# Optimization experiments

Measured on AMD Instinct MI355X. Metric: run time of the kernel, lower is better.

The kernel has to match this reference:

```python
import jax, jax.numpy as jnp
import numpy as np

TAU = 1.1      # LIF membrane time constant
ALPHA = 4.0    # sigmoid surrogate sharpness (spikingjelly default)
EPS = 1e-5     # BatchNorm eps
SCALE = 0.125  # attention scale


def lif(x, v_th):
    # Single-step LIF, v init 0, decay_input=True: v = x / tau; spike = H(v - v_th)
    # Straight-through: forward heaviside, backward sigmoid surrogate derivative.
    u = x / TAU - v_th
    sg = jax.nn.sigmoid(ALPHA * u)
    return sg + jax.lax.stop_gradient((u >= 0.0).astype(x.dtype) - sg)


def bn(x, gamma, beta):
    # BatchNorm1d in training mode on [B, C, N]: stats over (B, N) per channel
    mean = jnp.mean(x, axis=(0, 2), keepdims=True)
    var = jnp.var(x, axis=(0, 2), keepdims=True)
    return gamma[None, :, None] * (x - mean) * jax.lax.rsqrt(var + EPS) + beta[None, :, None]


def conv1x1(w, x):
    # Conv1d kernel_size=1: pointwise channel mix, x: [B,C,N], w: [O,C]
    return jnp.einsum('oc,bcn->bon', w, x)


def setup_inputs() -> dict:
    key = jax.random.key(0)
    B, C, N = 32, 512, 1024
    ks = jax.random.split(key, 6)
    s = 1.0 / np.sqrt(C)
    inp = {"x": jax.random.normal(ks[0], (B, C, N), jnp.float32)}
    for name, k in zip(["q", "k", "v", "proj"], ks[1:5]):
        inp[name + "_w"] = jax.random.uniform(k, (C, C), jnp.float32, -s, s)
        inp[name + "_gamma"] = jnp.ones((C,), jnp.float32)
        inp[name + "_beta"] = jnp.zeros((C,), jnp.float32)
    inp["proj_b"] = jax.random.uniform(ks[5], (C,), jnp.float32, -s, s)
    return inp


def reference(x, q_w, q_gamma, q_beta, k_w, k_gamma, k_beta, v_w, v_gamma, v_beta,
              proj_w, proj_b, proj_gamma, proj_beta):
    # x: [B, C, N]
    q = lif(bn(conv1x1(q_w, x), q_gamma, q_beta), 1.0)  # [B,C,N] spikes
    k = lif(bn(conv1x1(k_w, x), k_gamma, k_beta), 1.0)
    v = lif(bn(conv1x1(v_w, x), v_gamma, v_beta), 1.0)
    # linear (softmax-free) attention: kv[c,d] = sum_n k[n,c] v[n,d]
    kv = jnp.einsum('bcn,bdn->bcd', k, v)               # [B,C,C]
    attn = jnp.einsum('bcn,bcd->bdn', q, kv) * SCALE    # [B,C,N] (already transposed back)
    attn = lif(attn, 0.5)
    out = conv1x1(proj_w, attn) + proj_b[None, :, None]
    return lif(bn(out, proj_gamma, proj_beta), 1.0)
```

## Files before the change

### kernel.cpp

```cpp
#include <hip/hip_runtime.h>
#include <cstddef>


#define CC 512
#define BB 32
#define NN 1024

typedef __attribute__((ext_vector_type(4))) float v4f;
typedef __attribute__((ext_vector_type(2))) float v2f;
typedef __attribute__((ext_vector_type(4))) int v4i;
typedef __attribute__((ext_vector_type(8))) int v8i;
typedef unsigned char uchar;
typedef unsigned long long ull;

__device__ __forceinline__ uchar f2e4s(float v) {
  const uchar s = (v < 0.f) ? 0x80 : 0x00;
  float a = fabsf(v);
  if (a >= 464.f) return s | 0x7E;
  if (a < 0.015625f) {
    int q = (int)rintf(a * 512.f);
    return s | (uchar)q;
  }
  const int e = (int)((__float_as_uint(a) >> 23) & 0xFF) - 126;
  const float scale = __uint_as_float((unsigned)(4 - e + 127) << 23);
  const int q = (int)rintf(a * scale);
  int code = ((e - 1 + 7) << 3) + (q - 8);
  if (code > 0x7E) code = 0x7E;
  return s | (uchar)code;
}
__device__ __forceinline__ float e42f(uchar b) {
  const int e = (b >> 3) & 15, m = b & 7;
  const float mag = e ? __uint_as_float((unsigned)((e + 120) << 23) | ((unsigned)m << 20))
                      : (float)m * 0.001953125f;
  return (b & 0x80) ? -mag : mag;
}

__device__ __forceinline__ unsigned pk4_fp8(float a0, float a1, float a2, float a3) {
#if __has_builtin(__builtin_amdgcn_cvt_pk_fp8_f32)
  int r = __builtin_amdgcn_cvt_pk_fp8_f32(a0, a1, 0, false);
  r = __builtin_amdgcn_cvt_pk_fp8_f32(a2, a3, r, true);
  return (unsigned)r;
#else
  return (unsigned)f2e4s(a0) | ((unsigned)f2e4s(a1) << 8) |
         ((unsigned)f2e4s(a2) << 16) | ((unsigned)f2e4s(a3) << 24);
#endif
}
__device__ __forceinline__ uchar enc1(float v) {
#if __has_builtin(__builtin_amdgcn_cvt_pk_fp8_f32)
  return (uchar)(__builtin_amdgcn_cvt_pk_fp8_f32(v, v, 0, false) & 0xFF);
#else
  return f2e4s(v);
#endif
}
template <bool HI>
__device__ __forceinline__ v2f dec2(int src) {
#if __has_builtin(__builtin_amdgcn_cvt_pk_f32_fp8)
  return __builtin_amdgcn_cvt_pk_f32_fp8(src, HI);
#else
  v2f r;
  const int s = HI ? (src >> 16) : src;
  r[0] = e42f((uchar)s);
  r[1] = e42f((uchar)(s >> 8));
  return r;
#endif
}

__device__ __forceinline__ void gload16(const void* g, void* l) {
  __builtin_amdgcn_global_load_lds(
      (const __attribute__((address_space(1))) unsigned int*)g,
      (__attribute__((address_space(3))) unsigned int*)l, 16, 0, 0);
}

__device__ __forceinline__ float2 chan_affine(const float* __restrict__ P, int c,
                                              float g, float bt) {
  const float* pc = P + (size_t)c * 16;
  float S = 0.f, Q = 0.f;
#pragma unroll
  for (int t = 0; t < 8; t++) { S += pc[2 * t]; Q += pc[2 * t + 1]; }
  const float mean = S * (1.f / 32768.f);
  const float var = fmaxf(Q * (1.f / 32768.f) - mean * mean, 0.f);
  const float rinv = 1.f / sqrtf(var + 1e-5f);
  const float a = g * rinv;
  return make_float2(a, bt - mean * a);
}

template <int EPI>
__global__ __launch_bounds__(256) void gemm8(const uchar* __restrict__ A,
                                             const uchar* __restrict__ B,
                                             uchar* __restrict__ Cout,
                                             const float* __restrict__ bias,
                                             int M, int N, int K,
                                             long sA, long sB, long sC) {
  __shared__ __align__(16) uchar lds[32768];
  const int b = blockIdx.z;
  const uchar* Ab = A + (size_t)b * sA;
  const uchar* Bb = B + (size_t)b * sB;
  const int m0 = blockIdx.y * 128, n0 = blockIdx.x * 128;
  const int tid = threadIdx.x;
  const int wave = tid >> 6, lane = tid & 63;
  const int lrow = lane & 15, lquad = lane >> 4;
  const int wr = wave >> 1, wc = wave & 1;

  v4f acc[4][4];
#pragma unroll
  for (int i = 0; i < 4; i++)
#pragma unroll
    for (int j = 0; j < 4; j++) acc[i][j] = (v4f)0.f;

  const uchar* gA0 = Ab + (size_t)(m0 + 32 * wave + lrow) * K + lquad * 32;
  const uchar* gA1 = gA0 + (size_t)16 * K;
  const uchar* gB0 = Bb + (size_t)(n0 + 32 * wave + lrow) * K + lquad * 32;
  const uchar* gB1 = gB0 + (size_t)16 * K;
  uchar* lA0 = lds + (2 * wave) * 2048;
  uchar* lA1 = lA0 + 2048;
  uchar* lB0 = lds + 16384 + (2 * wave) * 2048;
  uchar* lB1 = lB0 + 2048;

  for (int k0 = 0; k0 < K; k0 += 128) {
    gload16(gA0, lA0);
    gload16(gA0 + 16, lA0 + 1024);
    gload16(gA1, lA1);
    gload16(gA1 + 16, lA1 + 1024);
    gload16(gB0, lB0);
    gload16(gB0 + 16, lB0 + 1024);
    gload16(gB1, lB1);
    gload16(gB1 + 16, lB1 + 1024);
    gA0 += 128; gA1 += 128; gB0 += 128; gB1 += 128;
    __syncthreads();
    const uchar* ra = lds + (size_t)(4 * wr) * 2048 + 16 * lane;
    const uchar* rb = lds + 16384 + (size_t)(4 * wc) * 2048 + 16 * lane;
    v8i af[4], bf[4];
#pragma unroll
    for (int i = 0; i < 4; i++) {
      const v4i lo = *(const v4i*)(ra + i * 2048);
      const v4i hi = *(const v4i*)(ra + i * 2048 + 1024);
      af[i][0] = lo[0]; af[i][1] = lo[1]; af[i][2] = lo[2]; af[i][3] = lo[3];
      af[i][4] = hi[0]; af[i][5] = hi[1]; af[i][6] = hi[2]; af[i][7] = hi[3];
    }
#pragma unroll
    for (int j = 0; j < 4; j++) {
      const v4i lo = *(const v4i*)(rb + j * 2048);
      const v4i hi = *(const v4i*)(rb + j * 2048 + 1024);
      bf[j][0] = lo[0]; bf[j][1] = lo[1]; bf[j][2] = lo[2]; bf[j][3] = lo[3];
      bf[j][4] = hi[0]; bf[j][5] = hi[1]; bf[j][6] = hi[2]; bf[j][7] = hi[3];
    }
#pragma unroll
    for (int i = 0; i < 4; i++)
#pragma unroll
      for (int j = 0; j < 4; j++)
        acc[i][j] = __builtin_amdgcn_mfma_scale_f32_16x16x128_f8f6f4(
            af[i], bf[j], acc[i][j], 0, 0, 0, 127, 0, 127);
    __syncthreads();
  }

  if (EPI == 3) {
#pragma unroll
    for (int mi = 0; mi < 4; mi++)
#pragma unroll
      for (int r = 0; r < 4; r++) {
        const float bi = bias[m0 + 64 * wr + 16 * mi + lquad * 4 + r];
#pragma unroll
        for (int ni = 0; ni < 4; ni++) acc[mi][ni][r] += bi;
      }
  }

#pragma unroll
  for (int mi = 0; mi < 4; mi++) {
    const int row0 = m0 + 64 * wr + 16 * mi + lquad * 4;
#pragma unroll
    for (int ni = 0; ni < 4; ni++) {
      const int col = n0 + 64 * wc + 16 * ni + lrow;
      uchar* cp = Cout + (size_t)b * sC + (size_t)row0 * N + col;
      if (EPI == 1) {
#pragma unroll
        for (int r = 0; r < 4; r++) {
          const float u = (acc[mi][ni][r] * 0.125f) / 1.1f - 0.5f;
          cp[(size_t)r * N] = (u >= 0.f) ? (uchar)0x38 : (uchar)0;
        }
      } else {
        const unsigned pk = pk4_fp8(acc[mi][ni][0], acc[mi][ni][1],
                                    acc[mi][ni][2], acc[mi][ni][3]);
#pragma unroll
        for (int r = 0; r < 4; r++) cp[(size_t)r * N] = (uchar)(pk >> (8 * r));
      }
    }
  }
}

__global__ __launch_bounds__(256) void stats_part8_k(const uchar* __restrict__ in,
                                                     float* __restrict__ P,
                                                     long bstride) {
  const int part = blockIdx.x, c = blockIdx.y;
  const int tid = threadIdx.x;
  const int bi = part * 4 + (tid >> 6);
  const int lane = tid & 63;
  const uchar* p = in + (size_t)bi * bstride + (size_t)c * 1024 + lane * 16;
  const uint4 u = *(const uint4*)p;
  const int w4[4] = {(int)u.x, (int)u.y, (int)u.z, (int)u.w};
  float s = 0.f, s2 = 0.f;
#pragma unroll
  for (int t = 0; t < 4; t++) {
    const v2f a = dec2<false>(w4[t]);
    const v2f bb = dec2<true>(w4[t]);
    s += (a[0] + a[1]) + (bb[0] + bb[1]);
    s2 += a[0] * a[0] + a[1] * a[1] + bb[0] * bb[0] + bb[1] * bb[1];
  }
#pragma unroll
  for (int off = 32; off > 0; off >>= 1) {
    s += __shfl_down(s, off, 64);
    s2 += __shfl_down(s2, off, 64);
  }
  __shared__ float rs[4], rq[4];
  const int w = tid >> 6;
  if (lane == 0) { rs[w] = s; rq[w] = s2; }
  __syncthreads();
  if (tid == 0) {
    float2 o = make_float2(rs[0] + rs[1] + rs[2] + rs[3],
                           rq[0] + rq[1] + rq[2] + rq[3]);
    *(float2*)(P + (size_t)(c * 8 + part) * 2) = o;
  }
}

__global__ __launch_bounds__(256) void apply_all_k(const uchar* __restrict__ qkv8,
                                                   uchar* __restrict__ q8,
                                                   uchar* __restrict__ k8,
                                                   uchar* __restrict__ v8,
                                                   const float* __restrict__ P,
                                                   const float* __restrict__ qg, const float* __restrict__ qb,
                                                   const float* __restrict__ kg, const float* __restrict__ kb,
                                                   const float* __restrict__ vg, const float* __restrict__ vb) {
  const int bid = blockIdx.x;
  const int tid = threadIdx.x;
  if (bid < 16384) {
    __shared__ uchar tile[32][33];
    const int nb = bid & 31, cb = (bid >> 5) & 15, b = bid >> 9;
    const int n0 = nb * 32, c0 = cb * 32;
    const uchar* in = qkv8 + (size_t)b * (1536 * 1024);
    const int cl = tid >> 3;
    const int n4 = (tid & 7) * 4;
    const int c = c0 + cl;
    const float2 ab = chan_affine(P, c, qg[c], qb[c]);
    const unsigned w = *(const unsigned*)(in + (size_t)c * 1024 + n0 + n4);
    const v2f a = dec2<false>((int)w);
    const v2f bb = dec2<true>((int)w);
    tile[cl][n4 + 0] = (ab.x * a[0] + ab.y >= 1.1f) ? (uchar)0x38 : (uchar)0;
    tile[cl][n4 + 1] = (ab.x * a[1] + ab.y >= 1.1f) ? (uchar)0x38 : (uchar)0;
    tile[cl][n4 + 2] = (ab.x * bb[0] + ab.y >= 1.1f) ? (uchar)0x38 : (uchar)0;
    tile[cl][n4 + 3] = (ab.x * bb[1] + ab.y >= 1.1f) ? (uchar)0x38 : (uchar)0;
    __syncthreads();
    uchar* out = q8 + (size_t)b * (NN * CC);
    const int nl = tid >> 3;
    const int cq = (tid & 7) * 4;
    uchar4 v;
    v.x = tile[cq][nl]; v.y = tile[cq + 1][nl];
    v.z = tile[cq + 2][nl]; v.w = tile[cq + 3][nl];
    *(uchar4*)(out + (size_t)(n0 + nl) * CC + c0 + cq) = v;
  } else {
    const int t0 = bid - 16384;
    const int sec = t0 >> 13;
    const int blk = t0 & 8191;
    const size_t t = (size_t)blk * 256 + tid;
    const size_t i = t * 8;
    const int b = (int)(i >> 19);
    const int rem = (int)(i & 524287);
    const int c = rem >> 10, n = rem & 1023;
    const int cg = 512 + 512 * sec + c;
    const float2 ab = chan_affine(P, cg, sec ? vg[c] : kg[c], sec ? vb[c] : kb[c]);
    const uchar* src = qkv8 + (size_t)b * (1536 * 1024) + (size_t)cg * 1024 + n;
    const uint2 u = *(const uint2*)src;
    ull packed = 0;
    {
      const v2f a = dec2<false>((int)u.x);
      const v2f bb = dec2<true>((int)u.x);
      const float f[4] = {a[0], a[1], bb[0], bb[1]};
#pragma unroll
      for (int j = 0; j < 4; j++)
        packed |= ((ab.x * f[j] + ab.y >= 1.1f) ? 0x38ull : 0ull) << (8 * j);
    }
    {
      const v2f a = dec2<false>((int)u.y);
      const v2f bb = dec2<true>((int)u.y);
      const float f[4] = {a[0], a[1], bb[0], bb[1]};
#pragma unroll
      for (int j = 0; j < 4; j++)
        packed |= ((ab.x * f[j] + ab.y >= 1.1f) ? 0x38ull : 0ull) << (8 * (4 + j));
    }
    uchar* dst = (sec ? v8 : k8) + (size_t)b * (CC * NN) + (size_t)c * 1024 + n;
    *(ull*)dst = packed;
  }
}

__global__ __launch_bounds__(256) void apply_final_k(const uchar* __restrict__ in,
                                                     float* __restrict__ outp,
                                                     const float* __restrict__ Pp,
                                                     const float* __restrict__ pg,
                                                     const float* __restrict__ pb) {
  const size_t idx = ((size_t)blockIdx.x * 256 + threadIdx.x) * 8;
  const int c = (int)((idx >> 10) & (CC - 1));
  const float2 ab = chan_affine(Pp, c, pg[c], pb[c]);
  const uint2 u = *(const uint2*)(in + idx);
  float of[8];
  {
    const v2f a = dec2<false>((int)u.x);
    const v2f bb = dec2<true>((int)u.x);
    of[0] = (ab.x * a[0] + ab.y >= 1.1f) ? 1.f : 0.f;
    of[1] = (ab.x * a[1] + ab.y >= 1.1f) ? 1.f : 0.f;
    of[2] = (ab.x * bb[0] + ab.y >= 1.1f) ? 1.f : 0.f;
    of[3] = (ab.x * bb[1] + ab.y >= 1.1f) ? 1.f : 0.f;
  }
  {
    const v2f a = dec2<false>((int)u.y);
    const v2f bb = dec2<true>((int)u.y);
    of[4] = (ab.x * a[0] + ab.y >= 1.1f) ? 1.f : 0.f;
    of[5] = (ab.x * a[1] + ab.y >= 1.1f) ? 1.f : 0.f;
    of[6] = (ab.x * bb[0] + ab.y >= 1.1f) ? 1.f : 0.f;
    of[7] = (ab.x * bb[1] + ab.y >= 1.1f) ? 1.f : 0.f;
  }
  float* op = outp + idx;
  *(float4*)op = make_float4(of[0], of[1], of[2], of[3]);
  *(float4*)(op + 4) = make_float4(of[4], of[5], of[6], of[7]);
}

__global__ __launch_bounds__(256) void prep_k(const float* __restrict__ x,
                                              const float* __restrict__ w0, const float* __restrict__ w1,
                                              const float* __restrict__ w2, const float* __restrict__ w3,
                                              uchar* __restrict__ xT8,
                                              uchar* __restrict__ o0, uchar* __restrict__ o1,
                                              uchar* __restrict__ o2, uchar* __restrict__ o3) {
  const int bid = blockIdx.x;
  const int tid = threadIdx.x;
  if (bid < 16384) {
    __shared__ uchar tile[32][33];
    const int nb = bid & 31, cb = (bid >> 5) & 15, b = bid >> 9;
    const int n0 = nb * 32, c0 = cb * 32;
    const float* in = x + (size_t)b * (CC * NN);
    const int tx = tid & 31, ty = tid >> 5;
#pragma unroll
    for (int i = 0; i < 32; i += 8) {
      tile[ty + i][tx] = enc1(in[(size_t)(c0 + ty + i) * NN + n0 + tx]);
    }
    __syncthreads();
    uchar* o = xT8 + (size_t)b * (NN * CC);
    const int nl = tid >> 3;
    const int cq = (tid & 7) * 4;
    uchar4 v;
    v.x = tile[cq][nl]; v.y = tile[cq + 1][nl];
    v.z = tile[cq + 2][nl]; v.w = tile[cq + 3][nl];
    *(uchar4*)(o + (size_t)(n0 + nl) * CC + c0 + cq) = v;
  } else {
    const int t = bid - 16384;
    const int mat = t >> 8, blk = t & 255;
    const float* src = (mat == 0) ? w0 : (mat == 1) ? w1 : (mat == 2) ? w2 : w3;
    uchar* dst = (mat == 0) ? o0 : (mat == 1) ? o1 : (mat == 2) ? o2 : o3;
    const int i = (blk * 256 + tid) * 4;
    float4 v = *(const float4*)(src + i);
    *(unsigned*)(dst + i) = pk4_fp8(v.x, v.y, v.z, v.w);
  }
}

extern "C" void kernel_launch(void* const* d_in, const int* in_sizes, int n_in,
                              void* d_out, int out_size, void* d_ws, size_t ws_size,
                              hipStream_t stream) {
  const float* x          = (const float*)d_in[0];
  const float* q_w        = (const float*)d_in[1];
  const float* q_gamma    = (const float*)d_in[2];
  const float* q_beta     = (const float*)d_in[3];
  const float* k_w        = (const float*)d_in[4];
  const float* k_gamma    = (const float*)d_in[5];
  const float* k_beta     = (const float*)d_in[6];
  const float* v_w        = (const float*)d_in[7];
  const float* v_gamma    = (const float*)d_in[8];
  const float* v_beta     = (const float*)d_in[9];
  const float* proj_w     = (const float*)d_in[10];
  const float* proj_gamma = (const float*)d_in[11];
  const float* proj_beta  = (const float*)d_in[12];
  const float* proj_b     = (const float*)d_in[13];

  char* base = (char*)d_ws;
  const size_t MB = 1u << 20;
  uchar*  xT8    = (uchar*)base;
  uchar*  qkv8   = (uchar*)(base + 16 * MB);
  uchar*  q8     = (uchar*)(base + 64 * MB);
  uchar*  k8     = (uchar*)(base + 80 * MB);
  uchar*  v8     = (uchar*)(base + 96 * MB);
  uchar*  kvT8   = (uchar*)(base + 112 * MB);
  uchar*  attnT8 = (uchar*)(base + 120 * MB);
  uchar*  outpre8= (uchar*)(base + 136 * MB);
  uchar*  wqkv8  = (uchar*)(base + 152 * MB);
  uchar*  wp8    = wqkv8 + 3 * CC * CC;
  float*  P      = (float*)(base + 154 * MB);
  float*  Pp     = P + 1536 * 16;
  float* dout = (float*)d_out;

  const long QKVL = (long)3 * CC * NN;
  const long NCL  = (long)NN * CC;
  const long CNL  = (long)CC * NN;
  const long KVL  = (long)CC * CC;

  prep_k<<<17408, 256, 0, stream>>>(x, q_w, k_w, v_w, proj_w, xT8,
                                    wqkv8, wqkv8 + CC * CC, wqkv8 + 2 * CC * CC, wp8);

  gemm8<2><<<dim3(NN / 128, 1536 / 128, BB), 256, 0, stream>>>(
      wqkv8, xT8, qkv8, nullptr, 1536, NN, CC, 0, NCL, QKVL);

  stats_part8_k<<<dim3(8, 1536), 256, 0, stream>>>(qkv8, P, QKVL);

  apply_all_k<<<32768, 256, 0, stream>>>(qkv8, q8, k8, v8, P,
                                         q_gamma, q_beta, k_gamma, k_beta,
                                         v_gamma, v_beta);

  gemm8<0><<<dim3(CC / 128, CC / 128, BB), 256, 0, stream>>>(
      v8, k8, kvT8, nullptr, CC, CC, NN, CNL, CNL, KVL);
  gemm8<1><<<dim3(CC / 128, NN / 128, BB), 256, 0, stream>>>(
      q8, kvT8, attnT8, nullptr, NN, CC, CC, NCL, KVL, NCL);
  gemm8<3><<<dim3(NN / 128, CC / 128, BB), 256, 0, stream>>>(
      wp8, attnT8, outpre8, proj_b, CC, NN, CC, 0, NCL, CNL);

  stats_part8_k<<<dim3(8, CC), 256, 0, stream>>>(outpre8, Pp, CNL);
  apply_final_k<<<8192, 256, 0, stream>>>(outpre8, dout, Pp, proj_gamma, proj_beta);
}
```

Before: 322.1 us.

## Add 256x256-tile ping-pong FP8 GEMM kernel for QKV, attention and projection GEMMs

Introduces a new gemm8p kernel with 512 threads and 256x256 output tiles. It double-buffers 128-wide K slices in 128 KB of LDS and interleaves global-to-LDS loads with MFMA phases, using barriers and priority bumps. Three of the four GEMMs now use it to raise data reuse per tile and overlap memory with compute. The larger LDS footprint and tiles cut occupancy and the number of workgroups, which may hurt load balance on the smaller GEMMs.

```diff
diff --git a/kernel.cpp b/kernel.cpp
--- a/kernel.cpp
+++ b/kernel.cpp
@@ -167,6 +167,145 @@
 #pragma unroll
   for (int mi = 0; mi < 4; mi++) {
     const int row0 = m0 + 64 * wr + 16 * mi + lquad * 4;
+#pragma unroll
+    for (int ni = 0; ni < 4; ni++) {
+      const int col = n0 + 64 * wc + 16 * ni + lrow;
+      uchar* cp = Cout + (size_t)b * sC + (size_t)row0 * N + col;
+      if (EPI == 1) {
+#pragma unroll
+        for (int r = 0; r < 4; r++) {
+          const float u = (acc[mi][ni][r] * 0.125f) / 1.1f - 0.5f;
+          cp[(size_t)r * N] = (u >= 0.f) ? (uchar)0x38 : (uchar)0;
+        }
+      } else {
+        const unsigned pk = pk4_fp8(acc[mi][ni][0], acc[mi][ni][1],
+                                    acc[mi][ni][2], acc[mi][ni][3]);
+#pragma unroll
+        for (int r = 0; r < 4; r++) cp[(size_t)r * N] = (uchar)(pk >> (8 * r));
+      }
+    }
+  }
+}
+
+template <int EPI>
+__global__ __launch_bounds__(512, 2) void gemm8p(const uchar* __restrict__ A,
+                                                 const uchar* __restrict__ B,
+                                                 uchar* __restrict__ Cout,
+                                                 const float* __restrict__ bias,
+                                                 int M, int N, int K,
+                                                 long sA, long sB, long sC) {
+  __shared__ __align__(16) uchar lds[131072];
+  const int b = blockIdx.z;
+  const uchar* Ab = A + (size_t)b * sA;
+  const uchar* Bb = B + (size_t)b * sB;
+  const int m0 = blockIdx.y * 256, n0 = blockIdx.x * 256;
+  const int tid = threadIdx.x;
+  const int wave = tid >> 6, lane = tid & 63;
+  const int lrow = lane & 15, lquad = lane >> 4;
+  const int wr = wave >> 2, wc = wave & 3;
+
+  v4f acc[8][4];
+#pragma unroll
+  for (int i = 0; i < 8; i++)
+#pragma unroll
+    for (int j = 0; j < 4; j++) acc[i][j] = (v4f)0.f;
+
+  const uchar* gA0 = Ab + (size_t)(m0 + 32 * wave + lrow) * K + lquad * 32;
+  const uchar* gA1 = gA0 + (size_t)16 * K;
+  const uchar* gB0 = Bb + (size_t)(n0 + 32 * wave + lrow) * K + lquad * 32;
+  const uchar* gB1 = gB0 + (size_t)16 * K;
+
+  const int NT = K >> 7;
+
+#define SSA_STAGE_A(bufi)                                   \
+  do {                                                      \
+    uchar* la = lds + (bufi) * 65536 + (2 * wave) * 2048;   \
+    gload16(gA0, la);                                       \
+    gload16(gA0 + 16, la + 1024);                           \
+    gload16(gA1, la + 2048);                                \
+    gload16(gA1 + 16, la + 3072);                           \
+  } while (0)
+#define SSA_STAGE_B(bufi)                                   \
+  do {                                                      \
+    uchar* lb = lds + (bufi) * 65536 + 32768 + (2 * wave) * 2048; \
+    gload16(gB0, lb);                                       \
+    gload16(gB0 + 16, lb + 1024);                           \
+    gload16(gB1, lb + 2048);                                \
+    gload16(gB1 + 16, lb + 3072);                           \
+  } while (0)
+
+  SSA_STAGE_A(0);
+  SSA_STAGE_B(0);
+  gA0 += 128; gA1 += 128; gB0 += 128; gB1 += 128;
+  asm volatile("s_waitcnt vmcnt(0)" ::: "memory");
+  __builtin_amdgcn_s_barrier();
+
+  for (int kt = 0; kt < NT; ++kt) {
+    const int cur = kt & 1;
+    const int nxt = cur ^ 1;
+    const bool more = (kt + 1 < NT);
+    const uchar* raA = lds + cur * 65536 + (8 * wr) * 2048 + 16 * lane;
+    const uchar* raB = lds + cur * 65536 + 32768 + (4 * wc) * 2048 + 16 * lane;
+    v8i bf[4];
+#pragma unroll
+    for (int p = 0; p < 4; ++p) {
+      const uchar* ra = raA + (2 * p) * 2048;
+      const v4i a0lo = *(const v4i*)(ra);
+      const v4i a0hi = *(const v4i*)(ra + 1024);
+      const v4i a1lo = *(const v4i*)(ra + 2048);
+      const v4i a1hi = *(const v4i*)(ra + 3072);
+      if (p == 0) {
+#pragma unroll
+        for (int j = 0; j < 4; ++j) {
+          const v4i lo = *(const v4i*)(raB + j * 2048);
+          const v4i hi = *(const v4i*)(raB + j * 2048 + 1024);
+          bf[j][0] = lo[0]; bf[j][1] = lo[1]; bf[j][2] = lo[2]; bf[j][3] = lo[3];
+          bf[j][4] = hi[0]; bf[j][5] = hi[1]; bf[j][6] = hi[2]; bf[j][7] = hi[3];
+        }
+        if (more) SSA_STAGE_A(nxt);
+      }
+      if (p == 1 && more) {
+        SSA_STAGE_B(nxt);
+        gA0 += 128; gA1 += 128; gB0 += 128; gB1 += 128;
+      }
+      __builtin_amdgcn_s_barrier();
+      asm volatile("s_waitcnt lgkmcnt(0)" ::: "memory");
+      __builtin_amdgcn_sched_barrier(0);
+      __builtin_amdgcn_s_setprio(1);
+      v8i af0, af1;
+      af0[0] = a0lo[0]; af0[1] = a0lo[1]; af0[2] = a0lo[2]; af0[3] = a0lo[3];
+      af0[4] = a0hi[0]; af0[5] = a0hi[1]; af0[6] = a0hi[2]; af0[7] = a0hi[3];
+      af1[0] = a1lo[0]; af1[1] = a1lo[1]; af1[2] = a1lo[2]; af1[3] = a1lo[3];
+      af1[4] = a1hi[0]; af1[5] = a1hi[1]; af1[6] = a1hi[2]; af1[7] = a1hi[3];
+#pragma unroll
+      for (int j = 0; j < 4; ++j) {
+        acc[2 * p][j] = __builtin_amdgcn_mfma_scale_f32_16x16x128_f8f6f4(
+            af0, bf[j], acc[2 * p][j], 0, 0, 0, 127, 0, 127);
+        acc[2 * p + 1][j] = __builtin_amdgcn_mfma_scale_f32_16x16x128_f8f6f4(
+            af1, bf[j], acc[2 * p + 1][j], 0, 0, 0, 127, 0, 127);
+      }
+      __builtin_amdgcn_s_setprio(0);
+      if (p == 3 && more) asm volatile("s_waitcnt vmcnt(0)" ::: "memory");
+      __builtin_amdgcn_s_barrier();
+    }
+  }
+#undef SSA_STAGE_A
+#undef SSA_STAGE_B
+
+  if (EPI == 3) {
+#pragma unroll
+    for (int mi = 0; mi < 8; mi++)
+#pragma unroll
+      for (int r = 0; r < 4; r++) {
+        const float bi = bias[m0 + 128 * wr + 16 * mi + lquad * 4 + r];
+#pragma unroll
+        for (int ni = 0; ni < 4; ni++) acc[mi][ni][r] += bi;
+      }
+  }
+
+#pragma unroll
+  for (int mi = 0; mi < 8; mi++) {
+    const int row0 = m0 + 128 * wr + 16 * mi + lquad * 4;
 #pragma unroll
     for (int ni = 0; ni < 4; ni++) {
       const int col = n0 + 64 * wc + 16 * ni + lrow;
@@ -400,7 +539,7 @@
   prep_k<<<17408, 256, 0, stream>>>(x, q_w, k_w, v_w, proj_w, xT8,
                                     wqkv8, wqkv8 + CC * CC, wqkv8 + 2 * CC * CC, wp8);
 
-  gemm8<2><<<dim3(NN / 128, 1536 / 128, BB), 256, 0, stream>>>(
+  gemm8p<2><<<dim3(NN / 256, 1536 / 256, BB), 512, 0, stream>>>(
       wqkv8, xT8, qkv8, nullptr, 1536, NN, CC, 0, NCL, QKVL);
 
   stats_part8_k<<<dim3(8, 1536), 256, 0, stream>>>(qkv8, P, QKVL);
@@ -411,9 +550,9 @@
 
   gemm8<0><<<dim3(CC / 128, CC / 128, BB), 256, 0, stream>>>(
       v8, k8, kvT8, nullptr, CC, CC, NN, CNL, CNL, KVL);
-  gemm8<1><<<dim3(CC / 128, NN / 128, BB), 256, 0, stream>>>(
+  gemm8p<1><<<dim3(CC / 256, NN / 256, BB), 512, 0, stream>>>(
       q8, kvT8, attnT8, nullptr, NN, CC, CC, NCL, KVL, NCL);
-  gemm8<3><<<dim3(NN / 128, CC / 128, BB), 256, 0, stream>>>(
+  gemm8p<3><<<dim3(NN / 256, CC / 256, BB), 512, 0, stream>>>(
       wp8, attnT8, outpre8, proj_b, CC, NN, CC, 0, NCL, CNL);
 
   stats_part8_k<<<dim3(8, CC), 256, 0, stream>>>(outpre8, Pp, CNL);
```

After: 313.1 us. -2.8%, faster.

## Double-buffer LDS tiles in FP8 GEMM with vmcnt-based prefetch and MFMA priority

Applied to the files above, without the earlier changes.

Converts the FP8 MFMA GEMM from a single-buffered load-sync-compute loop to a two-stage LDS ping-pong. The next K tile is prefetched while the current one is computed, with waits done through a partial s_waitcnt vmcnt instead of full __syncthreads. It also raises wave priority around the MFMA block. LDS per block doubles to 64 KB, which may reduce occupancy, and the hand-counted vmcnt relies on the exact number of outstanding loads.

```diff
diff --git a/kernel.cpp b/kernel.cpp
--- a/kernel.cpp
+++ b/kernel.cpp
@@ -85,13 +85,13 @@
 }
 
 template <int EPI>
-__global__ __launch_bounds__(256) void gemm8(const uchar* __restrict__ A,
-                                             const uchar* __restrict__ B,
-                                             uchar* __restrict__ Cout,
-                                             const float* __restrict__ bias,
-                                             int M, int N, int K,
-                                             long sA, long sB, long sC) {
-  __shared__ __align__(16) uchar lds[32768];
+__global__ __launch_bounds__(256) void gemm8q(const uchar* __restrict__ A,
+                                              const uchar* __restrict__ B,
+                                              uchar* __restrict__ Cout,
+                                              const float* __restrict__ bias,
+                                              int M, int N, int K,
+                                              long sA, long sB, long sC) {
+  __shared__ __align__(16) uchar lds[65536];
   const int b = blockIdx.z;
   const uchar* Ab = A + (size_t)b * sA;
   const uchar* Bb = B + (size_t)b * sB;
@@ -111,24 +111,37 @@
   const uchar* gA1 = gA0 + (size_t)16 * K;
   const uchar* gB0 = Bb + (size_t)(n0 + 32 * wave + lrow) * K + lquad * 32;
   const uchar* gB1 = gB0 + (size_t)16 * K;
-  uchar* lA0 = lds + (2 * wave) * 2048;
-  uchar* lA1 = lA0 + 2048;
-  uchar* lB0 = lds + 16384 + (2 * wave) * 2048;
-  uchar* lB1 = lB0 + 2048;
-
-  for (int k0 = 0; k0 < K; k0 += 128) {
-    gload16(gA0, lA0);
-    gload16(gA0 + 16, lA0 + 1024);
-    gload16(gA1, lA1);
-    gload16(gA1 + 16, lA1 + 1024);
-    gload16(gB0, lB0);
-    gload16(gB0 + 16, lB0 + 1024);
-    gload16(gB1, lB1);
-    gload16(gB1 + 16, lB1 + 1024);
+
+  const int NT = K >> 7;
+
+  auto stage = [&](int bufi) {
+    uchar* la = lds + bufi * 32768 + (2 * wave) * 2048;
+    uchar* lb = la + 16384;
+    gload16(gA0, la);
+    gload16(gA0 + 16, la + 1024);
+    gload16(gA1, la + 2048);
+    gload16(gA1 + 16, la + 3072);
+    gload16(gB0, lb);
+    gload16(gB0 + 16, lb + 1024);
+    gload16(gB1, lb + 2048);
+    gload16(gB1 + 16, lb + 3072);
     gA0 += 128; gA1 += 128; gB0 += 128; gB1 += 128;
-    __syncthreads();
-    const uchar* ra = lds + (size_t)(4 * wr) * 2048 + 16 * lane;
-    const uchar* rb = lds + 16384 + (size_t)(4 * wc) * 2048 + 16 * lane;
+  };
+
+  stage(0);
+  if (NT > 1) stage(1);
+
+  for (int kt = 0; kt < NT; ++kt) {
+    const int cur = kt & 1;
+    if (kt + 1 < NT) {
+      asm volatile("s_waitcnt vmcnt(8)" ::: "memory");
+    } else {
+      asm volatile("s_waitcnt vmcnt(0)" ::: "memory");
+    }
+    __builtin_amdgcn_s_barrier();
+
+    const uchar* ra = lds + cur * 32768 + (size_t)(4 * wr) * 2048 + 16 * lane;
+    const uchar* rb = lds + cur * 32768 + 16384 + (size_t)(4 * wc) * 2048 + 16 * lane;
     v8i af[4], bf[4];
 #pragma unroll
     for (int i = 0; i < 4; i++) {
@@ -144,13 +157,19 @@
       bf[j][0] = lo[0]; bf[j][1] = lo[1]; bf[j][2] = lo[2]; bf[j][3] = lo[3];
       bf[j][4] = hi[0]; bf[j][5] = hi[1]; bf[j][6] = hi[2]; bf[j][7] = hi[3];
     }
+    __builtin_amdgcn_s_setprio(1);
 #pragma unroll
     for (int i = 0; i < 4; i++)
 #pragma unroll
       for (int j = 0; j < 4; j++)
         acc[i][j] = __builtin_amdgcn_mfma_scale_f32_16x16x128_f8f6f4(
             af[i], bf[j], acc[i][j], 0, 0, 0, 127, 0, 127);
-    __syncthreads();
+    __builtin_amdgcn_s_setprio(0);
+
+    if (kt + 2 < NT) {
+      __builtin_amdgcn_s_barrier();
+      stage(cur);
+    }
   }
 
   if (EPI == 3) {
@@ -400,7 +419,7 @@
   prep_k<<<17408, 256, 0, stream>>>(x, q_w, k_w, v_w, proj_w, xT8,
                                     wqkv8, wqkv8 + CC * CC, wqkv8 + 2 * CC * CC, wp8);
 
-  gemm8<2><<<dim3(NN / 128, 1536 / 128, BB), 256, 0, stream>>>(
+  gemm8q<2><<<dim3(NN / 128, 1536 / 128, BB), 256, 0, stream>>>(
       wqkv8, xT8, qkv8, nullptr, 1536, NN, CC, 0, NCL, QKVL);
 
   stats_part8_k<<<dim3(8, 1536), 256, 0, stream>>>(qkv8, P, QKVL);
@@ -409,11 +428,11 @@
                                          q_gamma, q_beta, k_gamma, k_beta,
                                          v_gamma, v_beta);
 
-  gemm8<0><<<dim3(CC / 128, CC / 128, BB), 256, 0, stream>>>(
+  gemm8q<0><<<dim3(CC / 128, CC / 128, BB), 256, 0, stream>>>(
       v8, k8, kvT8, nullptr, CC, CC, NN, CNL, CNL, KVL);
-  gemm8<1><<<dim3(CC / 128, NN / 128, BB), 256, 0, stream>>>(
+  gemm8q<1><<<dim3(CC / 128, NN / 128, BB), 256, 0, stream>>>(
       q8, kvT8, attnT8, nullptr, NN, CC, CC, NCL, KVL, NCL);
-  gemm8<3><<<dim3(NN / 128, CC / 128, BB), 256, 0, stream>>>(
+  gemm8q<3><<<dim3(NN / 128, CC / 128, BB), 256, 0, stream>>>(
       wp8, attnT8, outpre8, proj_b, CC, NN, CC, 0, NCL, CNL);
 
   stats_part8_k<<<dim3(8, CC), 256, 0, stream>>>(outpre8, Pp, CNL);
```

After: 320.2 us. About the same (-0.6%).
